# Kernel tuning notes

Hardware: AMD Instinct MI355X
Metric: run time of the kernel (lower is better)

## Reference

```python
import jax, jax.numpy as jnp
import numpy as np

COMMITMENT_COST = 0.25
N_EMBED = 1024
EMB_DIM = 256

def setup_inputs() -> dict:
    key = jax.random.key(0)
    k1, k2 = jax.random.split(key)
    z = jax.random.normal(k1, (32, EMB_DIM, 32, 32), dtype=jnp.float32)
    # embedding.weight.data.uniform_(-1/n_embed, 1/n_embed)
    embedding = jax.random.uniform(k2, (N_EMBED, EMB_DIM), dtype=jnp.float32,
                                   minval=-1.0 / N_EMBED, maxval=1.0 / N_EMBED)
    return {"z": z, "embedding": embedding}

def reference(z, embedding):
    # NCHW -> NHWC
    zp = jnp.transpose(z, (0, 2, 3, 1))            # [B,H,W,D]
    in_shape = zp.shape
    flat = zp.reshape(-1, in_shape[-1])            # [N,D]
    # squared L2 distances (argmin equivalent to p=2 cdist argmin)
    d2 = (jnp.sum(flat * flat, axis=1, keepdims=True)
          - 2.0 * (flat @ embedding.T)
          + jnp.sum(embedding * embedding, axis=1))  # [N,K]
    idx = jnp.argmin(d2, axis=1)                   # [N]
    # one-hot @ codebook == direct gather
    z_quant = embedding[idx].reshape(in_shape)     # [B,H,W,D]
    codebook_loss = jnp.mean((z_quant - jax.lax.stop_gradient(zp)) ** 2)
    commitment_loss = jnp.mean((zp - jax.lax.stop_gradient(z_quant)) ** 2)
    loss = codebook_loss + COMMITMENT_COST * commitment_loss
    # straight-through estimator
    z_st = zp + jax.lax.stop_gradient(z_quant - zp)
    z_st = jnp.transpose(z_st, (0, 3, 1, 2))       # NHWC -> NCHW
    return (z_st, loss, codebook_loss, commitment_loss)
```

## Files before the change

### kernel.cpp

```cpp
#include <hip/hip_runtime.h>
#include <hip/hip_bf16.h>
#include <stdint.h>


typedef short v8s __attribute__((ext_vector_type(8)));
typedef float v4f __attribute__((ext_vector_type(4)));

__device__ inline unsigned short f2bf(float f) {
    uint32_t u = __float_as_uint(f);
    return (unsigned short)((u + 0x7fffu + ((u >> 16) & 1u)) >> 16);
}

__global__ __launch_bounds__(512) void k_prep_a(const float* __restrict__ z,
                                                unsigned short* __restrict__ Abf) {
    int tid = threadIdx.x;
    int b = blockIdx.x >> 4, hw0 = (blockIdx.x & 15) << 6;
    int t15 = tid & 15, dblk = tid >> 4;
    const float* zp = z + ((size_t)b << 18) + (size_t)(dblk << 3) * 1024 + hw0 + (t15 << 2);
    float4 L[8];
#pragma unroll
    for (int j = 0; j < 8; j++)
        L[j] = *(const float4*)(zp + (size_t)j * 1024);
    const float* Lf = (const float*)L;
    v8s* Aout = (v8s*)Abf + ((size_t)(b * 1024 + hw0 + (t15 << 2))) * 32 + dblk;
#pragma unroll
    for (int c = 0; c < 4; c++) {
        union { v8s v; unsigned short s[8]; } u;
#pragma unroll
        for (int j = 0; j < 8; j++) u.s[j] = f2bf(Lf[j * 4 + c]);
        Aout[(size_t)c * 32] = u.v;
    }
}

__global__ __launch_bounds__(256) void k_prep_e(const float* __restrict__ E,
                                                v8s* __restrict__ Esw,
                                                float* __restrict__ nE,
                                                float* __restrict__ accum) {
    __shared__ float Ef[16][264];
    int q = blockIdx.x, tid = threadIdx.x;
    const float4* Ein = (const float4*)(E + ((size_t)q << 12));
#pragma unroll
    for (int i = 0; i < 4; i++) {
        int f4 = i * 256 + tid;
        int row = f4 >> 6, c4 = (f4 & 63) << 2;
        *(float4*)&Ef[row][c4] = Ein[f4];
    }
    __syncthreads();
    {
        int c = tid >> 4, l = tid & 15;
        float s = 0.f;
#pragma unroll
        for (int j = 0; j < 16; j++) { float v = Ef[c][l + 16 * j]; s += v * v; }
#pragma unroll
        for (int off = 1; off < 16; off <<= 1) s += __shfl_xor(s, off);
        if (l == 0) nE[q * 16 + c] = 0.5f * s;
    }
#pragma unroll
    for (int i = 0; i < 2; i++) {
        int u = tid + i * 256;
        int um = u & 15, ug = (u >> 4) & 3, udc = (u >> 6) & 7;
        int d0 = udc * 32 + ug * 8;
        union { v8s v; unsigned short s[8]; } pk;
#pragma unroll
        for (int e = 0; e < 8; e++) pk.s[e] = f2bf(Ef[um][d0 + e]);
        Esw[((size_t)q << 9) + u] = pk.v;
    }
    if (q == 0 && tid == 0) accum[0] = 0.f;
}

__global__ __launch_bounds__(512) void k_main(
        const unsigned short* __restrict__ Abf,
        const v8s* __restrict__ Esw,
        const float* __restrict__ nE,
        const float* __restrict__ z,
        const float* __restrict__ E,
        float* __restrict__ out,
        float* __restrict__ accum) {
    __shared__ union {
        v8s    B[2][2048];
        float4 Eg4[2048];
    } S;
    __shared__ float nEl[1024];
    __shared__ int   idxLds[128];
    __shared__ float w8[8];

    int tid = threadIdx.x;
    int lane = tid & 63, w = tid >> 6;
    int g = lane >> 4, m = lane & 15;
    int R0 = blockIdx.x << 7;
    int b = R0 >> 10;

#pragma unroll
    for (int i = 0; i < 2; i++) nEl[tid + i * 512] = nE[tid + i * 512];

    v8s a[8];
    {
        const v8s* Ap = (const v8s*)Abf;
        int row = R0 + w * 16 + m;
#pragma unroll
        for (int dc = 0; dc < 8; dc++)
            a[dc] = Ap[(size_t)row * 32 + dc * 4 + g];
    }

#define STAGE(ch, buf)                                                        \
    {                                                                         \
        _Pragma("unroll")                                                     \
        for (int j = 0; j < 4; j++) {                                         \
            __builtin_amdgcn_global_load_lds(                                 \
                (const __attribute__((address_space(1))) void*)               \
                    (Esw + ((size_t)(ch) << 11) + (j << 9) + (w << 6) + lane),\
                (__attribute__((address_space(3))) void*)                     \
                    &S.B[buf][(j << 9) + (w << 6)],                           \
                16, 0, 0);                                                    \
        }                                                                     \
    }

    float best[4]; int bidx[4];
#pragma unroll
    for (int r = 0; r < 4; r++) { best[r] = 3.4e38f; bidx[r] = 0; }

    STAGE(0, 0);
#pragma unroll 1
    for (int ct = 0; ct < 16; ct++) {
        int cur = ct & 1;
        __syncthreads();
        if (ct < 15) STAGE(ct + 1, cur ^ 1);
        float ne[4];
#pragma unroll
        for (int t = 0; t < 4; t++) ne[t] = nEl[(ct << 6) + t * 16 + m];
        v4f acc[4];
#pragma unroll
        for (int t = 0; t < 4; t++) acc[t] = (v4f){0.f, 0.f, 0.f, 0.f};
#pragma unroll
        for (int dc = 0; dc < 8; dc++) {
#pragma unroll
            for (int t = 0; t < 4; t++) {
                v8s bf = S.B[cur][t * 512 + dc * 64 + g * 16 + m];
                acc[t] = __builtin_amdgcn_mfma_f32_16x16x32_bf16(a[dc], bf, acc[t], 0, 0, 0);
            }
        }
#pragma unroll
        for (int t = 0; t < 4; t++) {
            int code = (ct << 6) + t * 16 + m;
#pragma unroll
            for (int r = 0; r < 4; r++) {
                float s0 = ne[t] - acc[t][r];
                if (s0 < best[r]) { best[r] = s0; bidx[r] = code; }
            }
        }
    }

#pragma unroll
    for (int r = 0; r < 4; r++) {
        uint32_t sb = __float_as_uint(best[r]);
        sb = (sb & 0x80000000u) ? ~sb : (sb | 0x80000000u);
        unsigned long long pk = ((unsigned long long)sb << 32) | (uint32_t)bidx[r];
#pragma unroll
        for (int off = 1; off < 16; off <<= 1) {
            unsigned long long o = __shfl_xor(pk, off);
            if (o < pk) pk = o;
        }
        if (m == 0)
            idxLds[w * 16 + g * 4 + r] = (int)(pk & 0xffffffffu);
    }
    __syncthreads();

    float lsum = 0.f;
    const float* zb = z + ((size_t)b << 18);
    float* ob = out + ((size_t)b << 18);
    int hwl = tid & 31, dq0 = tid >> 5;
#pragma unroll 1
    for (int ph = 0; ph < 4; ph++) {
#pragma unroll
        for (int i = 0; i < 4; i++) {
            int row = w + (i << 3);
            int k = idxLds[(ph << 5) + row];
            float4 v = ((const float4*)(E + ((size_t)k << 8)))[lane];
            S.Eg4[(row << 6) + (lane ^ row)] = v;
        }
        __syncthreads();
        int hwp = (R0 & 1023) + (ph << 5) + hwl;
#pragma unroll
        for (int i = 0; i < 4; i++) {
            int dq = dq0 + (i << 4);
            float4 ev = S.Eg4[(hwl << 6) + (dq ^ hwl)];
            size_t o = ((size_t)dq << 12) + hwp;
            float z0 = zb[o], z1 = zb[o + 1024], z2 = zb[o + 2048], z3 = zb[o + 3072];
            ob[o] = ev.x; ob[o + 1024] = ev.y; ob[o + 2048] = ev.z; ob[o + 3072] = ev.w;
            float dx = ev.x - z0, dy = ev.y - z1, dz2 = ev.z - z2, dw = ev.w - z3;
            lsum += dx * dx + dy * dy + dz2 * dz2 + dw * dw;
        }
        __syncthreads();
    }
#pragma unroll
    for (int off = 1; off < 64; off <<= 1) lsum += __shfl_xor(lsum, off);
    if (lane == 0) w8[w] = lsum;
    __syncthreads();
    if (tid == 0) {
        float s = 0.f;
#pragma unroll
        for (int i = 0; i < 8; i++) s += w8[i];
        atomicAdd(accum, s);
    }
#undef STAGE
}

__global__ void k_loss(const float* __restrict__ accum, float* __restrict__ out) {
    if (threadIdx.x == 0) {
        float s = accum[0] * (1.0f / 8388608.0f);
        out[8388608] = 1.25f * s;
        out[8388609] = s;
        out[8388610] = s;
    }
}

extern "C" void kernel_launch(void* const* d_in, const int* in_sizes, int n_in,
                              void* d_out, int out_size, void* d_ws, size_t ws_size,
                              hipStream_t stream) {
    const float* z = (const float*)d_in[0];
    const float* E = (const float*)d_in[1];
    char* ws = (char*)d_ws;
    unsigned short* Abf   = (unsigned short*)(ws);
    v8s*            Esw   = (v8s*)(ws + 16777216);
    float*          nE    = (float*)(ws + 17301504);
    float*          accum = (float*)(ws + 17305600);
    float* out = (float*)d_out;

    hipLaunchKernelGGL(k_prep_e, dim3(64),  dim3(256), 0, stream, E, Esw, nE, accum);
    hipLaunchKernelGGL(k_prep_a, dim3(512), dim3(512), 0, stream, z, Abf);
    hipLaunchKernelGGL(k_main,   dim3(256), dim3(512), 0, stream,
                       Abf, Esw, nE, z, E, out, accum);
    hipLaunchKernelGGL(k_loss,   dim3(1),   dim3(64),  0, stream, accum, out);
}
```

Before: 127.9 us.

## Halve main-kernel block size to 64 rows and double grid, with 32-code tiles

The main distance/argmin kernel now runs 512 blocks of 256 threads, each covering 64 rows instead of 128, with launch bounds asking for two blocks per CU. The codebook is streamed in 32-code chunks over 32 iterations with a smaller double buffer, and B fragments are software-prefetched one step ahead of the MFMAs. This fills more CUs (256 blocks underfill a 256-CU part with one block each) and lowers register pressure. The cost is twice the total codebook traffic from L2 and more barriers per row.

```diff
diff --git a/kernel.cpp b/kernel.cpp
--- a/kernel.cpp
+++ b/kernel.cpp
@@ -68,7 +68,7 @@
     if (q == 0 && tid == 0) accum[0] = 0.f;
 }
 
-__global__ __launch_bounds__(512) void k_main(
+__global__ __launch_bounds__(256, 2) void k_main(
         const unsigned short* __restrict__ Abf,
         const v8s* __restrict__ Esw,
         const float* __restrict__ nE,
@@ -77,21 +77,21 @@
         float* __restrict__ out,
         float* __restrict__ accum) {
     __shared__ union {
-        v8s    B[2][2048];
+        v8s    B[2][1024];
         float4 Eg4[2048];
     } S;
     __shared__ float nEl[1024];
-    __shared__ int   idxLds[128];
-    __shared__ float w8[8];
+    __shared__ int   idxLds[64];
+    __shared__ float w4[4];
 
     int tid = threadIdx.x;
     int lane = tid & 63, w = tid >> 6;
     int g = lane >> 4, m = lane & 15;
-    int R0 = blockIdx.x << 7;
+    int R0 = blockIdx.x << 6;
     int b = R0 >> 10;
 
 #pragma unroll
-    for (int i = 0; i < 2; i++) nEl[tid + i * 512] = nE[tid + i * 512];
+    for (int i = 0; i < 4; i++) nEl[tid + i * 256] = nE[tid + i * 256];
 
     v8s a[8];
     {
@@ -108,9 +108,9 @@
         for (int j = 0; j < 4; j++) {                                         \
             __builtin_amdgcn_global_load_lds(                                 \
                 (const __attribute__((address_space(1))) void*)               \
-                    (Esw + ((size_t)(ch) << 11) + (j << 9) + (w << 6) + lane),\
+                    (Esw + ((size_t)(ch) << 10) + (j << 8) + (w << 6) + lane),\
                 (__attribute__((address_space(3))) void*)                     \
-                    &S.B[buf][(j << 9) + (w << 6)],                           \
+                    &S.B[buf][(j << 8) + (w << 6)],                           \
                 16, 0, 0);                                                    \
         }                                                                     \
     }
@@ -121,32 +121,34 @@
 
     STAGE(0, 0);
 #pragma unroll 1
-    for (int ct = 0; ct < 16; ct++) {
+    for (int ct = 0; ct < 32; ct++) {
         int cur = ct & 1;
         __syncthreads();
-        if (ct < 15) STAGE(ct + 1, cur ^ 1);
-        float ne[4];
-#pragma unroll
-        for (int t = 0; t < 4; t++) ne[t] = nEl[(ct << 6) + t * 16 + m];
-        v4f acc[4];
-#pragma unroll
-        for (int t = 0; t < 4; t++) acc[t] = (v4f){0.f, 0.f, 0.f, 0.f};
+        if (ct < 31) STAGE(ct + 1, cur ^ 1);
+        float ne0 = nEl[(ct << 5) + m];
+        float ne1 = nEl[(ct << 5) + 16 + m];
+        v4f acc0 = {0.f, 0.f, 0.f, 0.f}, acc1 = {0.f, 0.f, 0.f, 0.f};
+        int base = g * 16 + m;
+        v8s bf0 = S.B[cur][base];
+        v8s bf1 = S.B[cur][512 + base];
 #pragma unroll
         for (int dc = 0; dc < 8; dc++) {
-#pragma unroll
-            for (int t = 0; t < 4; t++) {
-                v8s bf = S.B[cur][t * 512 + dc * 64 + g * 16 + m];
-                acc[t] = __builtin_amdgcn_mfma_f32_16x16x32_bf16(a[dc], bf, acc[t], 0, 0, 0);
+            v8s nf0, nf1;
+            if (dc < 7) {
+                nf0 = S.B[cur][(dc + 1) * 64 + base];
+                nf1 = S.B[cur][512 + (dc + 1) * 64 + base];
             }
-        }
-#pragma unroll
-        for (int t = 0; t < 4; t++) {
-            int code = (ct << 6) + t * 16 + m;
-#pragma unroll
-            for (int r = 0; r < 4; r++) {
-                float s0 = ne[t] - acc[t][r];
-                if (s0 < best[r]) { best[r] = s0; bidx[r] = code; }
-            }
+            acc0 = __builtin_amdgcn_mfma_f32_16x16x32_bf16(a[dc], bf0, acc0, 0, 0, 0);
+            acc1 = __builtin_amdgcn_mfma_f32_16x16x32_bf16(a[dc], bf1, acc1, 0, 0, 0);
+            bf0 = nf0; bf1 = nf1;
+        }
+        int code = (ct << 5) + m;
+#pragma unroll
+        for (int r = 0; r < 4; r++) {
+            float s0 = ne0 - acc0[r];
+            if (s0 < best[r]) { best[r] = s0; bidx[r] = code; }
+            float s1 = ne1 - acc1[r];
+            if (s1 < best[r]) { best[r] = s1; bidx[r] = code + 16; }
         }
     }
 
@@ -170,10 +172,10 @@
     float* ob = out + ((size_t)b << 18);
     int hwl = tid & 31, dq0 = tid >> 5;
 #pragma unroll 1
-    for (int ph = 0; ph < 4; ph++) {
-#pragma unroll
-        for (int i = 0; i < 4; i++) {
-            int row = w + (i << 3);
+    for (int ph = 0; ph < 2; ph++) {
+#pragma unroll
+        for (int i = 0; i < 8; i++) {
+            int row = w + (i << 2);
             int k = idxLds[(ph << 5) + row];
             float4 v = ((const float4*)(E + ((size_t)k << 8)))[lane];
             S.Eg4[(row << 6) + (lane ^ row)] = v;
@@ -181,8 +183,8 @@
         __syncthreads();
         int hwp = (R0 & 1023) + (ph << 5) + hwl;
 #pragma unroll
-        for (int i = 0; i < 4; i++) {
-            int dq = dq0 + (i << 4);
+        for (int i = 0; i < 8; i++) {
+            int dq = dq0 + (i << 3);
             float4 ev = S.Eg4[(hwl << 6) + (dq ^ hwl)];
             size_t o = ((size_t)dq << 12) + hwp;
             float z0 = zb[o], z1 = zb[o + 1024], z2 = zb[o + 2048], z3 = zb[o + 3072];
@@ -194,14 +196,9 @@
     }
 #pragma unroll
     for (int off = 1; off < 64; off <<= 1) lsum += __shfl_xor(lsum, off);
-    if (lane == 0) w8[w] = lsum;
+    if (lane == 0) w4[w] = lsum;
     __syncthreads();
-    if (tid == 0) {
-        float s = 0.f;
-#pragma unroll
-        for (int i = 0; i < 8; i++) s += w8[i];
-        atomicAdd(accum, s);
-    }
+    if (tid == 0) atomicAdd(accum, w4[0] + w4[1] + w4[2] + w4[3]);
 #undef STAGE
 }
 
@@ -228,7 +225,7 @@
 
     hipLaunchKernelGGL(k_prep_e, dim3(64),  dim3(256), 0, stream, E, Esw, nE, accum);
     hipLaunchKernelGGL(k_prep_a, dim3(512), dim3(512), 0, stream, z, Abf);
-    hipLaunchKernelGGL(k_main,   dim3(256), dim3(512), 0, stream,
+    hipLaunchKernelGGL(k_main,   dim3(512), dim3(256), 0, stream,
                        Abf, Esw, nE, z, E, out, accum);
     hipLaunchKernelGGL(k_loss,   dim3(1),   dim3(64),  0, stream, accum, out);
 }
```

Result: slower. 136.8 us (+7.0%).

## Split codebook search across blocks and move gather/output to separate kernel

Applied to the files above, without the earlier changes.

The distance/argmin kernel now tiles 256 rows by 256 codes per block, with each wave holding four row sub-tiles so each staged codebook fragment feeds four MFMAs. The four code-slices write packed (score,index) candidates to a workspace buffer. A new kernel reduces those candidates, then gathers codewords, writes the NCHW output and accumulates the loss. This spreads the search over more blocks and increases B-operand reuse. The cost is an extra launch, a candidate round trip through global memory, and higher register pressure from the a[4][8] and 4x4 best arrays.

```diff
diff --git a/kernel.cpp b/kernel.cpp
--- a/kernel.cpp
+++ b/kernel.cpp
@@ -68,141 +68,155 @@
     if (q == 0 && tid == 0) accum[0] = 0.f;
 }
 
-__global__ __launch_bounds__(512) void k_main(
+__global__ __launch_bounds__(256, 2) void k_main(
         const unsigned short* __restrict__ Abf,
         const v8s* __restrict__ Esw,
         const float* __restrict__ nE,
-        const float* __restrict__ z,
-        const float* __restrict__ E,
-        float* __restrict__ out,
-        float* __restrict__ accum) {
-    __shared__ union {
-        v8s    B[2][2048];
-        float4 Eg4[2048];
-    } S;
-    __shared__ float nEl[1024];
-    __shared__ int   idxLds[128];
-    __shared__ float w8[8];
+        unsigned long long* __restrict__ cand) {
+    __shared__ v8s B[2][2048];
+    __shared__ float nEl[256];
 
     int tid = threadIdx.x;
     int lane = tid & 63, w = tid >> 6;
     int g = lane >> 4, m = lane & 15;
-    int R0 = blockIdx.x << 7;
-    int b = R0 >> 10;
-
-#pragma unroll
-    for (int i = 0; i < 2; i++) nEl[tid + i * 512] = nE[tid + i * 512];
-
-    v8s a[8];
+    int cs = blockIdx.x & 3;
+    int R0 = (blockIdx.x >> 2) << 8;
+    int C0 = cs << 8;
+
+    nEl[tid] = nE[C0 + tid];
+
+    v8s a[4][8];
     {
         const v8s* Ap = (const v8s*)Abf;
-        int row = R0 + w * 16 + m;
-#pragma unroll
-        for (int dc = 0; dc < 8; dc++)
-            a[dc] = Ap[(size_t)row * 32 + dc * 4 + g];
+#pragma unroll
+        for (int s = 0; s < 4; s++) {
+            int row = R0 + (w << 6) + (s << 4) + m;
+#pragma unroll
+            for (int dc = 0; dc < 8; dc++)
+                a[s][dc] = Ap[(size_t)row * 32 + dc * 4 + g];
+        }
     }
 
 #define STAGE(ch, buf)                                                        \
     {                                                                         \
         _Pragma("unroll")                                                     \
-        for (int j = 0; j < 4; j++) {                                         \
+        for (int j = 0; j < 8; j++) {                                         \
             __builtin_amdgcn_global_load_lds(                                 \
                 (const __attribute__((address_space(1))) void*)               \
-                    (Esw + ((size_t)(ch) << 11) + (j << 9) + (w << 6) + lane),\
+                    (Esw + ((size_t)(C0 + (ch) * 64) << 5) + (j << 8)         \
+                         + (w << 6) + lane),                                  \
                 (__attribute__((address_space(3))) void*)                     \
-                    &S.B[buf][(j << 9) + (w << 6)],                           \
+                    &B[buf][(j << 8) + (w << 6)],                             \
                 16, 0, 0);                                                    \
         }                                                                     \
     }
 
-    float best[4]; int bidx[4];
-#pragma unroll
-    for (int r = 0; r < 4; r++) { best[r] = 3.4e38f; bidx[r] = 0; }
+    float best[4][4]; int bidx[4][4];
+#pragma unroll
+    for (int s = 0; s < 4; s++)
+#pragma unroll
+        for (int r = 0; r < 4; r++) { best[s][r] = 3.4e38f; bidx[s][r] = 0; }
 
     STAGE(0, 0);
 #pragma unroll 1
-    for (int ct = 0; ct < 16; ct++) {
+    for (int ct = 0; ct < 4; ct++) {
         int cur = ct & 1;
         __syncthreads();
-        if (ct < 15) STAGE(ct + 1, cur ^ 1);
-        float ne[4];
-#pragma unroll
-        for (int t = 0; t < 4; t++) ne[t] = nEl[(ct << 6) + t * 16 + m];
-        v4f acc[4];
-#pragma unroll
-        for (int t = 0; t < 4; t++) acc[t] = (v4f){0.f, 0.f, 0.f, 0.f};
-#pragma unroll
-        for (int dc = 0; dc < 8; dc++) {
-#pragma unroll
-            for (int t = 0; t < 4; t++) {
-                v8s bf = S.B[cur][t * 512 + dc * 64 + g * 16 + m];
-                acc[t] = __builtin_amdgcn_mfma_f32_16x16x32_bf16(a[dc], bf, acc[t], 0, 0, 0);
+        if (ct < 3) STAGE(ct + 1, cur ^ 1);
+#pragma unroll
+        for (int t = 0; t < 4; t++) {
+            float ne = nEl[(ct << 6) + (t << 4) + m];
+            v4f acc[4];
+#pragma unroll
+            for (int s = 0; s < 4; s++) acc[s] = (v4f){0.f, 0.f, 0.f, 0.f};
+#pragma unroll
+            for (int dc = 0; dc < 8; dc++) {
+                v8s bf = B[cur][(t << 9) + (dc << 6) + (g << 4) + m];
+                acc[0] = __builtin_amdgcn_mfma_f32_16x16x32_bf16(a[0][dc], bf, acc[0], 0, 0, 0);
+                acc[1] = __builtin_amdgcn_mfma_f32_16x16x32_bf16(a[1][dc], bf, acc[1], 0, 0, 0);
+                acc[2] = __builtin_amdgcn_mfma_f32_16x16x32_bf16(a[2][dc], bf, acc[2], 0, 0, 0);
+                acc[3] = __builtin_amdgcn_mfma_f32_16x16x32_bf16(a[3][dc], bf, acc[3], 0, 0, 0);
             }
-        }
-#pragma unroll
-        for (int t = 0; t < 4; t++) {
-            int code = (ct << 6) + t * 16 + m;
-#pragma unroll
-            for (int r = 0; r < 4; r++) {
-                float s0 = ne[t] - acc[t][r];
-                if (s0 < best[r]) { best[r] = s0; bidx[r] = code; }
+            int code = C0 + (ct << 6) + (t << 4) + m;
+#pragma unroll
+            for (int s = 0; s < 4; s++)
+#pragma unroll
+                for (int r = 0; r < 4; r++) {
+                    float sc = ne - acc[s][r];
+                    if (sc < best[s][r]) { best[s][r] = sc; bidx[s][r] = code; }
+                }
+        }
+    }
+
+#pragma unroll
+    for (int s = 0; s < 4; s++)
+#pragma unroll
+        for (int r = 0; r < 4; r++) {
+            uint32_t sb = __float_as_uint(best[s][r]);
+            sb = (sb & 0x80000000u) ? ~sb : (sb | 0x80000000u);
+            unsigned long long pk = ((unsigned long long)sb << 32) | (uint32_t)bidx[s][r];
+#pragma unroll
+            for (int off = 1; off < 16; off <<= 1) {
+                unsigned long long o = __shfl_xor(pk, off);
+                if (o < pk) pk = o;
             }
-        }
-    }
-
-#pragma unroll
-    for (int r = 0; r < 4; r++) {
-        uint32_t sb = __float_as_uint(best[r]);
-        sb = (sb & 0x80000000u) ? ~sb : (sb | 0x80000000u);
-        unsigned long long pk = ((unsigned long long)sb << 32) | (uint32_t)bidx[r];
-#pragma unroll
-        for (int off = 1; off < 16; off <<= 1) {
-            unsigned long long o = __shfl_xor(pk, off);
-            if (o < pk) pk = o;
-        }
-        if (m == 0)
-            idxLds[w * 16 + g * 4 + r] = (int)(pk & 0xffffffffu);
-    }
-    __syncthreads();
-
+            if (m == 0)
+                cand[((size_t)cs << 15) + R0 + (w << 6) + (s << 4) + (g << 2) + r] = pk;
+        }
+#undef STAGE
+}
+
+__global__ __launch_bounds__(256) void k_out(const float* __restrict__ z,
+                                             const float* __restrict__ E,
+                                             const unsigned long long* __restrict__ cand,
+                                             float* __restrict__ out,
+                                             float* __restrict__ accum) {
+    __shared__ float4 Eg4[2048];
+    __shared__ int    kk[32];
+    __shared__ float  w4[4];
+    int bid = blockIdx.x;
+    int b = bid >> 5, hw0 = (bid & 31) << 5;
+    int tid = threadIdx.x;
+    int lane = tid & 63, w = tid >> 6;
+    if (tid < 32) {
+        int n = b * 1024 + hw0 + tid;
+        unsigned long long bv = cand[n];
+#pragma unroll
+        for (int s = 1; s < 4; s++) {
+            unsigned long long v = cand[((size_t)s << 15) + n];
+            if (v < bv) bv = v;
+        }
+        kk[tid] = (int)(bv & 0xffffffffu);
+    }
+    __syncthreads();
+#pragma unroll
+    for (int i = 0; i < 8; i++) {
+        int row = w + (i << 2);
+        int k = kk[row];
+        float4 v = ((const float4*)(E + ((size_t)k << 8)))[lane];
+        Eg4[(row << 6) + (lane ^ row)] = v;
+    }
+    __syncthreads();
     float lsum = 0.f;
     const float* zb = z + ((size_t)b << 18);
     float* ob = out + ((size_t)b << 18);
     int hwl = tid & 31, dq0 = tid >> 5;
-#pragma unroll 1
-    for (int ph = 0; ph < 4; ph++) {
-#pragma unroll
-        for (int i = 0; i < 4; i++) {
-            int row = w + (i << 3);
-            int k = idxLds[(ph << 5) + row];
-            float4 v = ((const float4*)(E + ((size_t)k << 8)))[lane];
-            S.Eg4[(row << 6) + (lane ^ row)] = v;
-        }
-        __syncthreads();
-        int hwp = (R0 & 1023) + (ph << 5) + hwl;
-#pragma unroll
-        for (int i = 0; i < 4; i++) {
-            int dq = dq0 + (i << 4);
-            float4 ev = S.Eg4[(hwl << 6) + (dq ^ hwl)];
-            size_t o = ((size_t)dq << 12) + hwp;
-            float z0 = zb[o], z1 = zb[o + 1024], z2 = zb[o + 2048], z3 = zb[o + 3072];
-            ob[o] = ev.x; ob[o + 1024] = ev.y; ob[o + 2048] = ev.z; ob[o + 3072] = ev.w;
-            float dx = ev.x - z0, dy = ev.y - z1, dz2 = ev.z - z2, dw = ev.w - z3;
-            lsum += dx * dx + dy * dy + dz2 * dz2 + dw * dw;
-        }
-        __syncthreads();
+    int hwp = hw0 + hwl;
+#pragma unroll
+    for (int i = 0; i < 8; i++) {
+        int dq = dq0 + (i << 3);
+        float4 ev = Eg4[(hwl << 6) + (dq ^ hwl)];
+        size_t o = ((size_t)dq << 12) + hwp;
+        float z0 = zb[o], z1 = zb[o + 1024], z2 = zb[o + 2048], z3 = zb[o + 3072];
+        ob[o] = ev.x; ob[o + 1024] = ev.y; ob[o + 2048] = ev.z; ob[o + 3072] = ev.w;
+        float dx = ev.x - z0, dy = ev.y - z1, dz2 = ev.z - z2, dw = ev.w - z3;
+        lsum += dx * dx + dy * dy + dz2 * dz2 + dw * dw;
     }
 #pragma unroll
     for (int off = 1; off < 64; off <<= 1) lsum += __shfl_xor(lsum, off);
-    if (lane == 0) w8[w] = lsum;
-    __syncthreads();
-    if (tid == 0) {
-        float s = 0.f;
-#pragma unroll
-        for (int i = 0; i < 8; i++) s += w8[i];
-        atomicAdd(accum, s);
-    }
-#undef STAGE
+    if (lane == 0) w4[w] = lsum;
+    __syncthreads();
+    if (tid == 0) atomicAdd(accum, w4[0] + w4[1] + w4[2] + w4[3]);
 }
 
 __global__ void k_loss(const float* __restrict__ accum, float* __restrict__ out) {
@@ -220,15 +234,16 @@
     const float* z = (const float*)d_in[0];
     const float* E = (const float*)d_in[1];
     char* ws = (char*)d_ws;
-    unsigned short* Abf   = (unsigned short*)(ws);
-    v8s*            Esw   = (v8s*)(ws + 16777216);
-    float*          nE    = (float*)(ws + 17301504);
-    float*          accum = (float*)(ws + 17305600);
+    unsigned short*     Abf   = (unsigned short*)(ws);
+    v8s*                Esw   = (v8s*)(ws + 16777216);
+    float*              nE    = (float*)(ws + 17301504);
+    unsigned long long* cand  = (unsigned long long*)(ws + 17305600);
+    float*              accum = (float*)(ws + 18354176);
     float* out = (float*)d_out;
 
-    hipLaunchKernelGGL(k_prep_e, dim3(64),  dim3(256), 0, stream, E, Esw, nE, accum);
-    hipLaunchKernelGGL(k_prep_a, dim3(512), dim3(512), 0, stream, z, Abf);
-    hipLaunchKernelGGL(k_main,   dim3(256), dim3(512), 0, stream,
-                       Abf, Esw, nE, z, E, out, accum);
-    hipLaunchKernelGGL(k_loss,   dim3(1),   dim3(64),  0, stream, accum, out);
-}
+    hipLaunchKernelGGL(k_prep_e, dim3(64),   dim3(256), 0, stream, E, Esw, nE, accum);
+    hipLaunchKernelGGL(k_prep_a, dim3(512),  dim3(512), 0, stream, z, Abf);
+    hipLaunchKernelGGL(k_main,   dim3(512),  dim3(256), 0, stream, Abf, Esw, nE, cand);
+    hipLaunchKernelGGL(k_out,    dim3(1024), dim3(256), 0, stream, z, E, cand, out, accum);
+    hipLaunchKernelGGL(k_loss,   dim3(1),    dim3(64),  0, stream, accum, out);
+}
```

Result: slower. 135.5 us (+5.9%).
